# Kernel optimization log

Measured on AMD Instinct MI355X. Metric: run time of the kernel, lower is better.

Reference implementation:

```python
import jax, jax.numpy as jnp
import numpy as np

NEG = -1000000000.0

def setup_inputs() -> dict:
    key = jax.random.key(0)
    kq, kk, kv = jax.random.split(key, 3)
    B, S, D = 4, 4096, 128
    q = jax.random.normal(kq, (B, S, D), dtype=jnp.float32)
    k = jax.random.normal(kk, (B, S, D), dtype=jnp.float32)
    v = jax.random.normal(kv, (B, S, D), dtype=jnp.float32)
    return {"q": q, "k": k, "v": v, "window_size": 128}

def reference(q, k, v, window_size):
    B, S, D = q.shape
    q = q / jnp.sqrt(jnp.asarray(D, q.dtype))
    # banded mask: keep |i-j| <= window_size-1 (tril(w-1) & triu(-(w-1)))
    idx = jnp.arange(S)
    band = jnp.abs(idx[:, None] - idx[None, :]) <= (window_size - 1)  # [S,S]
    scores = jnp.einsum('bqd,bkd->bqk', q, k)
    scores = jnp.where(band[None, :, :], scores, NEG)
    weights = jax.nn.softmax(scores, axis=-1)
    return jnp.einsum('bqk,bkd->bqd', weights, v)
```

## Files before the change

### kernel.cpp

```cpp
#include <hip/hip_runtime.h>

#define S_LEN  4096
#define D_DIM  128
#define MQ     64
#define KT     64
#define NBATCH 4

#define QS_STR 136
#define KS_STR 136
#define VT_STR 72
#define PS_STR 72

#define OFF_K0 8704
#define OFF_K1 17408
#define OFF_V0 26112
#define OFF_V1 36480
#define OFF_P  46848
#define LDS_TOT 56064

typedef __bf16 bf16x8 __attribute__((ext_vector_type(8)));
typedef float  f32x4  __attribute__((ext_vector_type(4)));
typedef unsigned short u16x4 __attribute__((ext_vector_type(4)));
typedef unsigned short u16x8 __attribute__((ext_vector_type(8)));

__device__ __forceinline__ unsigned short f2bf(float f) {
  return __builtin_bit_cast(unsigned short, static_cast<__bf16>(f));
}
__device__ __forceinline__ float fexp2(float x) { return __builtin_amdgcn_exp2f(x); }
__device__ __forceinline__ bf16x8 ld8(const unsigned short* p) {
  return __builtin_bit_cast(bf16x8, *(const u16x8*)p);
}
__device__ __forceinline__ f32x4 mfma16(bf16x8 a, bf16x8 b, f32x4 c) {
  return __builtin_amdgcn_mfma_f32_16x16x32_bf16(a, b, c, 0, 0, 0);
}

__global__ __launch_bounds__(512, 2)
void swa_fwd(const float* __restrict__ Qg, const float* __restrict__ Kg,
             const float* __restrict__ Vg, float* __restrict__ Og)
{
  __shared__ __align__(16) unsigned short lds[LDS_TOT];

  const int tid  = threadIdx.x;
  const int g    = (blockIdx.x & 7) * 32 + (blockIdx.x >> 3);
  const int b    = g >> 6;
  const int q0   = (g & 63) * MQ;
  const size_t base = (size_t)b * S_LEN * D_DIM;

  const int lane = tid & 63;
  const int wv   = tid >> 6;
  const int grp  = wv >> 2;
  const int wvg  = wv & 3;
  const int tg   = tid & 255;
  const int quad = lane >> 4;
  const int l15  = lane & 15;

  unsigned short* lds_q  = lds;
  unsigned short* lds_k  = lds + (grp ? OFF_K1 : OFF_K0);
  unsigned short* lds_vt = lds + (grp ? OFF_V1 : OFF_V0);
  unsigned short* pw     = lds + OFF_P + wv * 16 * PS_STR;

  const int t_lo = (q0 >= 128) ? 0 : (2 - (q0 >> 6));
  const int t_hi = (4032 - q0 >= 128) ? 4 : (2 + ((4032 - q0) >> 6));

  const int t_beg = grp ? 3 : t_lo;
  const int ntile = grp ? (t_hi - 2) : (3 - t_lo);

  const int vd0 = (tg & 31) * 4;
  const int vk0 = (tg >> 5) * 8;

  f32x4 qreg[8], kreg[8], vreg[8];
  if (grp == 0) {
    const float* gq = Qg + base + (size_t)q0 * D_DIM;
#pragma unroll
    for (int j = 0; j < 8; ++j) qreg[j] = *(const f32x4*)(gq + j * 1024 + tg * 4);
  }
  int kb = q0 + (t_beg - 2) * KT;
  if (ntile > 0) {
    const float* gk = Kg + base + (size_t)kb * D_DIM;
    const float* gv = Vg + base + (size_t)kb * D_DIM;
#pragma unroll
    for (int j = 0; j < 8; ++j) kreg[j] = *(const f32x4*)(gk + j * 1024 + tg * 4);
#pragma unroll
    for (int kk = 0; kk < 8; ++kk)
      vreg[kk] = *(const f32x4*)(gv + (size_t)(vk0 + kk) * D_DIM + vd0);
  }

  for (int s = tg; s < 16 * VT_STR; s += 256)
    lds_vt[128 * VT_STR + s] = (s < VT_STR) ? (unsigned short)0x3F80 : (unsigned short)0;

  if (grp == 0) {
    const float qsc = 1.4426950408889634f * 0.08838834764831845f;
#pragma unroll
    for (int j = 0; j < 8; ++j) {
      const int f = j * 1024 + tg * 4;
      u16x4 y;
#pragma unroll
      for (int e = 0; e < 4; ++e) y[e] = f2bf(qreg[j][e] * qsc);
      *(u16x4*)&lds_q[(f >> 7) * QS_STR + (f & 127)] = y;
    }
  }
  if (ntile > 0) {
#pragma unroll
    for (int j = 0; j < 8; ++j) {
      const int f = j * 1024 + tg * 4;
      u16x4 y;
#pragma unroll
      for (int e = 0; e < 4; ++e) y[e] = f2bf(kreg[j][e]);
      *(u16x4*)&lds_k[(f >> 7) * KS_STR + (f & 127)] = y;
    }
#pragma unroll
    for (int e = 0; e < 4; ++e) {
      u16x8 y;
#pragma unroll
      for (int kk = 0; kk < 8; ++kk) y[kk] = f2bf(vreg[kk][e]);
      *(u16x8*)&lds_vt[(vd0 + e) * VT_STR + vk0] = y;
    }
  }
  __syncthreads();

  bf16x8 aq[4];
#pragma unroll
  for (int ks = 0; ks < 4; ++ks)
    aq[ks] = ld8(&lds_q[(wvg * 16 + l15) * QS_STR + ks * 32 + quad * 8]);

  f32x4 acc[9];
#pragma unroll
  for (int d = 0; d < 9; ++d) acc[d] = (f32x4){0.f, 0.f, 0.f, 0.f};

  for (int step = 0; step < 3; ++step) {
    const int t = t_beg + step;
    const bool cur = (step < ntile);
    const bool nxt = (step + 1 < ntile);

    if (nxt) {
      const float* gk = Kg + base + (size_t)(kb + KT) * D_DIM;
      const float* gv = Vg + base + (size_t)(kb + KT) * D_DIM;
#pragma unroll
      for (int j = 0; j < 8; ++j) kreg[j] = *(const f32x4*)(gk + j * 1024 + tg * 4);
#pragma unroll
      for (int kk = 0; kk < 8; ++kk)
        vreg[kk] = *(const f32x4*)(gv + (size_t)(vk0 + kk) * D_DIM + vd0);
    }

    if (cur) {
      int cbLo = 0, cbHi = 3;
      if (t == 0) cbLo = wvg;
      if (t == 4) cbHi = wvg;
      f32x4 sc[4];
      __builtin_amdgcn_s_setprio(1);
#pragma unroll
      for (int cb = 0; cb < 4; ++cb) {
        if (cb < cbLo || cb > cbHi) {
          sc[cb] = (f32x4){-1.0e30f, -1.0e30f, -1.0e30f, -1.0e30f};
          continue;
        }
        f32x4 a = (f32x4){0.f, 0.f, 0.f, 0.f};
#pragma unroll
        for (int ks = 0; ks < 4; ++ks) {
          const bf16x8 kf = ld8(&lds_k[(cb * 16 + l15) * KS_STR + ks * 32 + quad * 8]);
          a = mfma16(aq[ks], kf, a);
        }
        sc[cb] = a;
      }
      __builtin_amdgcn_s_setprio(0);

      if (t == 0 || t == 4) {
        const int off = (t - 2) * KT;
#pragma unroll
        for (int cb = 0; cb < 4; ++cb)
#pragma unroll
          for (int r = 0; r < 4; ++r) {
            const int delta = (wvg * 16 + quad * 4 + r) - (off + cb * 16 + l15);
            if (delta > 127 || delta < -127) sc[cb][r] = -1.0e30f;
          }
      }

#pragma unroll
      for (int cb = 0; cb < 4; ++cb)
#pragma unroll
        for (int r = 0; r < 4; ++r)
          sc[cb][r] = fexp2(sc[cb][r]);

#pragma unroll
      for (int cb = 0; cb < 4; ++cb)
#pragma unroll
        for (int r = 0; r < 4; ++r)
          pw[(quad * 4 + r) * PS_STR + cb * 16 + l15] = f2bf(sc[cb][r]);

      __builtin_amdgcn_s_setprio(1);
#pragma unroll
      for (int ks2 = 0; ks2 < 2; ++ks2) {
        const bf16x8 pf = ld8(&pw[l15 * PS_STR + ks2 * 32 + quad * 8]);
#pragma unroll
        for (int d = 0; d < 9; ++d) {
          const bf16x8 vf = ld8(&lds_vt[(d * 16 + l15) * VT_STR + ks2 * 32 + quad * 8]);
          acc[d] = mfma16(pf, vf, acc[d]);
        }
      }
      __builtin_amdgcn_s_setprio(0);
    }

    __syncthreads();
    if (nxt) {
#pragma unroll
      for (int j = 0; j < 8; ++j) {
        const int f = j * 1024 + tg * 4;
        u16x4 y;
#pragma unroll
        for (int e = 0; e < 4; ++e) y[e] = f2bf(kreg[j][e]);
        *(u16x4*)&lds_k[(f >> 7) * KS_STR + (f & 127)] = y;
      }
#pragma unroll
      for (int e = 0; e < 4; ++e) {
        u16x8 y;
#pragma unroll
        for (int kk = 0; kk < 8; ++kk) y[kk] = f2bf(vreg[kk][e]);
        *(u16x8*)&lds_vt[(vd0 + e) * VT_STR + vk0] = y;
      }
    }
    __syncthreads();
    kb += KT;
  }

  float* msc = (float*)lds;
  if (grp == 1) {
    float* p = msc + (wvg * 64 + lane) * 37;
#pragma unroll
    for (int d = 0; d < 9; ++d)
#pragma unroll
      for (int r = 0; r < 4; ++r) p[d * 4 + r] = acc[d][r];
  }
  __syncthreads();
  if (grp == 0) {
    const float* p = msc + (wvg * 64 + lane) * 37;
#pragma unroll
    for (int d = 0; d < 9; ++d)
#pragma unroll
      for (int r = 0; r < 4; ++r) acc[d][r] += p[d * 4 + r];

    float inv[4];
#pragma unroll
    for (int r = 0; r < 4; ++r) {
      const float lr = __shfl(acc[8][r], lane & 48, 64);
      inv[r] = 1.0f / lr;
    }
    float* go = Og + base + (size_t)q0 * D_DIM;
#pragma unroll
    for (int d = 0; d < 8; ++d)
#pragma unroll
      for (int r = 0; r < 4; ++r)
        go[(size_t)(wvg * 16 + quad * 4 + r) * D_DIM + d * 16 + l15] = acc[d][r] * inv[r];
  }
}

extern "C" void kernel_launch(void* const* d_in, const int* in_sizes, int n_in,
                              void* d_out, int out_size, void* d_ws, size_t ws_size,
                              hipStream_t stream) {
  const float* q = (const float*)d_in[0];
  const float* k = (const float*)d_in[1];
  const float* v = (const float*)d_in[2];
  float* o = (float*)d_out;
  dim3 grid(NBATCH * (S_LEN / MQ));
  dim3 block(512);
  swa_fwd<<<grid, block, 0, stream>>>(q, k, v, o);
}
```

Before: 86.01 us.

## Split into bf16 prep pass and small-block attention kernel reading from global

Result: slower. 98.47 us (+14.5%).

```diff
diff --git a/kernel.cpp b/kernel.cpp
--- a/kernel.cpp
+++ b/kernel.cpp
@@ -2,21 +2,12 @@
 
 #define S_LEN  4096
 #define D_DIM  128
-#define MQ     64
-#define KT     64
 #define NBATCH 4
-
-#define QS_STR 136
-#define KS_STR 136
-#define VT_STR 72
 #define PS_STR 72
 
-#define OFF_K0 8704
-#define OFF_K1 17408
-#define OFF_V0 26112
-#define OFF_V1 36480
-#define OFF_P  46848
-#define LDS_TOT 56064
+#define WS_Q 0
+#define WS_K 4194304
+#define WS_V 8388608
 
 typedef __bf16 bf16x8 __attribute__((ext_vector_type(8)));
 typedef float  f32x4  __attribute__((ext_vector_type(4)));
@@ -34,205 +25,167 @@
   return __builtin_amdgcn_mfma_f32_16x16x32_bf16(a, b, c, 0, 0, 0);
 }
 
-__global__ __launch_bounds__(512, 2)
-void swa_fwd(const float* __restrict__ Qg, const float* __restrict__ Kg,
-             const float* __restrict__ Vg, float* __restrict__ Og)
+__global__ __launch_bounds__(256, 4)
+void prep(const float* __restrict__ Q, const float* __restrict__ K,
+          const float* __restrict__ V, unsigned short* __restrict__ Qb,
+          unsigned short* __restrict__ Kb, unsigned short* __restrict__ Vt)
 {
-  __shared__ __align__(16) unsigned short lds[LDS_TOT];
+  __shared__ __align__(16) float lv[64 * 136];
+  const int t  = threadIdx.x;
+  const int b  = blockIdx.x >> 6;
+  const int s0 = (blockIdx.x & 63) * 64;
+  const size_t ibase = (size_t)b * S_LEN * D_DIM + (size_t)s0 * D_DIM;
+  const float qsc = 1.4426950408889634f * 0.08838834764831845f;
+
+#pragma unroll
+  for (int j = 0; j < 8; ++j) {
+    const int f = j * 1024 + t * 4;
+    const f32x4 xq = *(const f32x4*)(Q + ibase + f);
+    const f32x4 xk = *(const f32x4*)(K + ibase + f);
+    const f32x4 xv = *(const f32x4*)(V + ibase + f);
+    u16x4 yq, yk;
+#pragma unroll
+    for (int e = 0; e < 4; ++e) { yq[e] = f2bf(xq[e] * qsc); yk[e] = f2bf(xk[e]); }
+    *(u16x4*)(Qb + ibase + f) = yq;
+    *(u16x4*)(Kb + ibase + f) = yk;
+    *(f32x4*)&lv[(f >> 7) * 136 + (f & 127)] = xv;
+  }
+  __syncthreads();
+
+  const int d  = t >> 1;
+  const int ch = (t & 1) * 32;
+  unsigned short* out = Vt + ((size_t)b * 144 + d) * S_LEN + s0 + ch;
+#pragma unroll
+  for (int kk = 0; kk < 4; ++kk) {
+    u16x8 y;
+#pragma unroll
+    for (int e = 0; e < 8; ++e) y[e] = f2bf(lv[(ch + kk * 8 + e) * 136 + d]);
+    *(u16x8*)(out + kk * 8) = y;
+  }
+  if (t < 128) {
+    const int row = 128 + (t >> 3), k8 = (t & 7) * 8;
+    const unsigned short vv = (row == 128) ? (unsigned short)0x3F80 : (unsigned short)0;
+    u16x8 y;
+#pragma unroll
+    for (int e = 0; e < 8; ++e) y[e] = vv;
+    *(u16x8*)(Vt + ((size_t)b * 144 + row) * S_LEN + s0 + k8) = y;
+  }
+}
+
+__global__ __launch_bounds__(128, 2)
+void swa_fwd(const unsigned short* __restrict__ Qb, const unsigned short* __restrict__ Kb,
+             const unsigned short* __restrict__ Vt, float* __restrict__ Og)
+{
+  __shared__ __align__(16) unsigned short lds_p[2 * 16 * PS_STR];
+  __shared__ __align__(16) float msc[64 * 37];
 
   const int tid  = threadIdx.x;
-  const int g    = (blockIdx.x & 7) * 32 + (blockIdx.x >> 3);
-  const int b    = g >> 6;
-  const int q0   = (g & 63) * MQ;
-  const size_t base = (size_t)b * S_LEN * D_DIM;
-
   const int lane = tid & 63;
-  const int wv   = tid >> 6;
-  const int grp  = wv >> 2;
-  const int wvg  = wv & 3;
-  const int tg   = tid & 255;
+  const int part = tid >> 6;
   const int quad = lane >> 4;
   const int l15  = lane & 15;
 
-  unsigned short* lds_q  = lds;
-  unsigned short* lds_k  = lds + (grp ? OFF_K1 : OFF_K0);
-  unsigned short* lds_vt = lds + (grp ? OFF_V1 : OFF_V0);
-  unsigned short* pw     = lds + OFF_P + wv * 16 * PS_STR;
-
-  const int t_lo = (q0 >= 128) ? 0 : (2 - (q0 >> 6));
-  const int t_hi = (4032 - q0 >= 128) ? 4 : (2 + ((4032 - q0) >> 6));
-
-  const int t_beg = grp ? 3 : t_lo;
-  const int ntile = grp ? (t_hi - 2) : (3 - t_lo);
-
-  const int vd0 = (tg & 31) * 4;
-  const int vk0 = (tg >> 5) * 8;
-
-  f32x4 qreg[8], kreg[8], vreg[8];
-  if (grp == 0) {
-    const float* gq = Qg + base + (size_t)q0 * D_DIM;
-#pragma unroll
-    for (int j = 0; j < 8; ++j) qreg[j] = *(const f32x4*)(gq + j * 1024 + tg * 4);
-  }
-  int kb = q0 + (t_beg - 2) * KT;
-  if (ntile > 0) {
-    const float* gk = Kg + base + (size_t)kb * D_DIM;
-    const float* gv = Vg + base + (size_t)kb * D_DIM;
-#pragma unroll
-    for (int j = 0; j < 8; ++j) kreg[j] = *(const f32x4*)(gk + j * 1024 + tg * 4);
-#pragma unroll
-    for (int kk = 0; kk < 8; ++kk)
-      vreg[kk] = *(const f32x4*)(gv + (size_t)(vk0 + kk) * D_DIM + vd0);
-  }
-
-  for (int s = tg; s < 16 * VT_STR; s += 256)
-    lds_vt[128 * VT_STR + s] = (s < VT_STR) ? (unsigned short)0x3F80 : (unsigned short)0;
-
-  if (grp == 0) {
-    const float qsc = 1.4426950408889634f * 0.08838834764831845f;
-#pragma unroll
-    for (int j = 0; j < 8; ++j) {
-      const int f = j * 1024 + tg * 4;
-      u16x4 y;
-#pragma unroll
-      for (int e = 0; e < 4; ++e) y[e] = f2bf(qreg[j][e] * qsc);
-      *(u16x4*)&lds_q[(f >> 7) * QS_STR + (f & 127)] = y;
-    }
-  }
-  if (ntile > 0) {
-#pragma unroll
-    for (int j = 0; j < 8; ++j) {
-      const int f = j * 1024 + tg * 4;
-      u16x4 y;
-#pragma unroll
-      for (int e = 0; e < 4; ++e) y[e] = f2bf(kreg[j][e]);
-      *(u16x4*)&lds_k[(f >> 7) * KS_STR + (f & 127)] = y;
-    }
-#pragma unroll
-    for (int e = 0; e < 4; ++e) {
-      u16x8 y;
-#pragma unroll
-      for (int kk = 0; kk < 8; ++kk) y[kk] = f2bf(vreg[kk][e]);
-      *(u16x8*)&lds_vt[(vd0 + e) * VT_STR + vk0] = y;
-    }
+  const int g  = (blockIdx.x & 7) * 128 + (blockIdx.x >> 3);
+  const int b  = g >> 8;
+  const int qs = (g & 255) * 16;
+
+  const unsigned short* Qg = Qb + (size_t)b * S_LEN * D_DIM;
+  const unsigned short* Kg = Kb + (size_t)b * S_LEN * D_DIM;
+  const unsigned short* Vg = Vt + (size_t)b * 144 * S_LEN;
+
+  int lo_key = qs - 127; if (lo_key < 0) lo_key = 0;
+  int hi_key = qs + 142; if (hi_key > S_LEN - 1) hi_key = S_LEN - 1;
+  const int kb_lo = lo_key & ~63;
+  const int nt = (((hi_key & ~63) - kb_lo) >> 6) + 1;
+  const int n0 = nt >> 1;
+  const int tb = part ? n0 : 0;
+  const int te = part ? nt : n0;
+
+  bf16x8 aq[4];
+#pragma unroll
+  for (int ks = 0; ks < 4; ++ks)
+    aq[ks] = ld8(Qg + (size_t)(qs + l15) * D_DIM + ks * 32 + quad * 8);
+
+  f32x4 acc[9];
+#pragma unroll
+  for (int d = 0; d < 9; ++d) acc[d] = (f32x4){0.f, 0.f, 0.f, 0.f};
+
+  unsigned short* pw = lds_p + part * 16 * PS_STR;
+
+  for (int ti = tb; ti < te; ++ti) {
+    const int kb = kb_lo + ti * 64;
+
+    f32x4 sc[4];
+    __builtin_amdgcn_s_setprio(1);
+#pragma unroll
+    for (int cb = 0; cb < 4; ++cb) {
+      const int kbc = kb + cb * 16;
+      if (kbc + 15 < qs - 127 || kbc > qs + 142) {
+        sc[cb] = (f32x4){-1.0e30f, -1.0e30f, -1.0e30f, -1.0e30f};
+        continue;
+      }
+      f32x4 a = (f32x4){0.f, 0.f, 0.f, 0.f};
+#pragma unroll
+      for (int ks = 0; ks < 4; ++ks) {
+        const bf16x8 kf = ld8(Kg + (size_t)(kbc + l15) * D_DIM + ks * 32 + quad * 8);
+        a = mfma16(aq[ks], kf, a);
+      }
+      sc[cb] = a;
+    }
+    __builtin_amdgcn_s_setprio(0);
+
+    bf16x8 vfr[9];
+#pragma unroll
+    for (int d = 0; d < 9; ++d)
+      vfr[d] = ld8(Vg + (size_t)(d * 16 + l15) * S_LEN + kb + quad * 8);
+
+    if (kb < qs - 112 || kb > qs + 64) {
+#pragma unroll
+      for (int cb = 0; cb < 4; ++cb)
+#pragma unroll
+        for (int r = 0; r < 4; ++r) {
+          const int delta = (qs + quad * 4 + r) - (kb + cb * 16 + l15);
+          if (delta > 127 || delta < -127) sc[cb][r] = -1.0e30f;
+        }
+    }
+
+#pragma unroll
+    for (int cb = 0; cb < 4; ++cb)
+#pragma unroll
+      for (int r = 0; r < 4; ++r)
+        sc[cb][r] = fexp2(sc[cb][r]);
+
+#pragma unroll
+    for (int cb = 0; cb < 4; ++cb)
+#pragma unroll
+      for (int r = 0; r < 4; ++r)
+        pw[(quad * 4 + r) * PS_STR + cb * 16 + l15] = f2bf(sc[cb][r]);
+
+    __builtin_amdgcn_s_setprio(1);
+    {
+      const bf16x8 pf0 = ld8(&pw[l15 * PS_STR + quad * 8]);
+#pragma unroll
+      for (int d = 0; d < 9; ++d) acc[d] = mfma16(pf0, vfr[d], acc[d]);
+      const bf16x8 pf1 = ld8(&pw[l15 * PS_STR + 32 + quad * 8]);
+#pragma unroll
+      for (int d = 0; d < 9; ++d) {
+        const bf16x8 vf = ld8(Vg + (size_t)(d * 16 + l15) * S_LEN + kb + 32 + quad * 8);
+        acc[d] = mfma16(pf1, vf, acc[d]);
+      }
+    }
+    __builtin_amdgcn_s_setprio(0);
+  }
+
+  if (part == 1) {
+    float* p = msc + lane * 37;
+#pragma unroll
+    for (int d = 0; d < 9; ++d)
+#pragma unroll
+      for (int r = 0; r < 4; ++r) p[d * 4 + r] = acc[d][r];
   }
   __syncthreads();
-
-  bf16x8 aq[4];
-#pragma unroll
-  for (int ks = 0; ks < 4; ++ks)
-    aq[ks] = ld8(&lds_q[(wvg * 16 + l15) * QS_STR + ks * 32 + quad * 8]);
-
-  f32x4 acc[9];
-#pragma unroll
-  for (int d = 0; d < 9; ++d) acc[d] = (f32x4){0.f, 0.f, 0.f, 0.f};
-
-  for (int step = 0; step < 3; ++step) {
-    const int t = t_beg + step;
-    const bool cur = (step < ntile);
-    const bool nxt = (step + 1 < ntile);
-
-    if (nxt) {
-      const float* gk = Kg + base + (size_t)(kb + KT) * D_DIM;
-      const float* gv = Vg + base + (size_t)(kb + KT) * D_DIM;
-#pragma unroll
-      for (int j = 0; j < 8; ++j) kreg[j] = *(const f32x4*)(gk + j * 1024 + tg * 4);
-#pragma unroll
-      for (int kk = 0; kk < 8; ++kk)
-        vreg[kk] = *(const f32x4*)(gv + (size_t)(vk0 + kk) * D_DIM + vd0);
-    }
-
-    if (cur) {
-      int cbLo = 0, cbHi = 3;
-      if (t == 0) cbLo = wvg;
-      if (t == 4) cbHi = wvg;
-      f32x4 sc[4];
-      __builtin_amdgcn_s_setprio(1);
-#pragma unroll
-      for (int cb = 0; cb < 4; ++cb) {
-        if (cb < cbLo || cb > cbHi) {
-          sc[cb] = (f32x4){-1.0e30f, -1.0e30f, -1.0e30f, -1.0e30f};
-          continue;
-        }
-        f32x4 a = (f32x4){0.f, 0.f, 0.f, 0.f};
-#pragma unroll
-        for (int ks = 0; ks < 4; ++ks) {
-          const bf16x8 kf = ld8(&lds_k[(cb * 16 + l15) * KS_STR + ks * 32 + quad * 8]);
-          a = mfma16(aq[ks], kf, a);
-        }
-        sc[cb] = a;
-      }
-      __builtin_amdgcn_s_setprio(0);
-
-      if (t == 0 || t == 4) {
-        const int off = (t - 2) * KT;
-#pragma unroll
-        for (int cb = 0; cb < 4; ++cb)
-#pragma unroll
-          for (int r = 0; r < 4; ++r) {
-            const int delta = (wvg * 16 + quad * 4 + r) - (off + cb * 16 + l15);
-            if (delta > 127 || delta < -127) sc[cb][r] = -1.0e30f;
-          }
-      }
-
-#pragma unroll
-      for (int cb = 0; cb < 4; ++cb)
-#pragma unroll
-        for (int r = 0; r < 4; ++r)
-          sc[cb][r] = fexp2(sc[cb][r]);
-
-#pragma unroll
-      for (int cb = 0; cb < 4; ++cb)
-#pragma unroll
-        for (int r = 0; r < 4; ++r)
-          pw[(quad * 4 + r) * PS_STR + cb * 16 + l15] = f2bf(sc[cb][r]);
-
-      __builtin_amdgcn_s_setprio(1);
-#pragma unroll
-      for (int ks2 = 0; ks2 < 2; ++ks2) {
-        const bf16x8 pf = ld8(&pw[l15 * PS_STR + ks2 * 32 + quad * 8]);
-#pragma unroll
-        for (int d = 0; d < 9; ++d) {
-          const bf16x8 vf = ld8(&lds_vt[(d * 16 + l15) * VT_STR + ks2 * 32 + quad * 8]);
-          acc[d] = mfma16(pf, vf, acc[d]);
-        }
-      }
-      __builtin_amdgcn_s_setprio(0);
-    }
-
-    __syncthreads();
-    if (nxt) {
-#pragma unroll
-      for (int j = 0; j < 8; ++j) {
-        const int f = j * 1024 + tg * 4;
-        u16x4 y;
-#pragma unroll
-        for (int e = 0; e < 4; ++e) y[e] = f2bf(kreg[j][e]);
-        *(u16x4*)&lds_k[(f >> 7) * KS_STR + (f & 127)] = y;
-      }
-#pragma unroll
-      for (int e = 0; e < 4; ++e) {
-        u16x8 y;
-#pragma unroll
-        for (int kk = 0; kk < 8; ++kk) y[kk] = f2bf(vreg[kk][e]);
-        *(u16x8*)&lds_vt[(vd0 + e) * VT_STR + vk0] = y;
-      }
-    }
-    __syncthreads();
-    kb += KT;
-  }
-
-  float* msc = (float*)lds;
-  if (grp == 1) {
-    float* p = msc + (wvg * 64 + lane) * 37;
-#pragma unroll
-    for (int d = 0; d < 9; ++d)
-#pragma unroll
-      for (int r = 0; r < 4; ++r) p[d * 4 + r] = acc[d][r];
-  }
-  __syncthreads();
-  if (grp == 0) {
-    const float* p = msc + (wvg * 64 + lane) * 37;
+  if (part == 0) {
+    const float* p = msc + lane * 37;
 #pragma unroll
     for (int d = 0; d < 9; ++d)
 #pragma unroll
@@ -244,12 +197,12 @@
       const float lr = __shfl(acc[8][r], lane & 48, 64);
       inv[r] = 1.0f / lr;
     }
-    float* go = Og + base + (size_t)q0 * D_DIM;
+    float* go = Og + ((size_t)b * S_LEN + qs) * D_DIM;
 #pragma unroll
     for (int d = 0; d < 8; ++d)
 #pragma unroll
       for (int r = 0; r < 4; ++r)
-        go[(size_t)(wvg * 16 + quad * 4 + r) * D_DIM + d * 16 + l15] = acc[d][r] * inv[r];
+        go[(size_t)(quad * 4 + r) * D_DIM + d * 16 + l15] = acc[d][r] * inv[r];
   }
 }
 
@@ -260,7 +213,10 @@
   const float* k = (const float*)d_in[1];
   const float* v = (const float*)d_in[2];
   float* o = (float*)d_out;
-  dim3 grid(NBATCH * (S_LEN / MQ));
-  dim3 block(512);
-  swa_fwd<<<grid, block, 0, stream>>>(q, k, v, o);
-}
+  unsigned short* qb = (unsigned short*)((char*)d_ws + WS_Q);
+  unsigned short* kb = (unsigned short*)((char*)d_ws + WS_K);
+  unsigned short* vt = (unsigned short*)((char*)d_ws + WS_V);
+
+  prep<<<dim3(NBATCH * (S_LEN / 64)), dim3(256), 0, stream>>>(q, k, v, qb, kb, vt);
+  swa_fwd<<<dim3(NBATCH * (S_LEN / 16)), dim3(128), 0, stream>>>(qb, kb, vt, o);
+}
```

## Double-buffer K/V tiles in swizzled LDS and load Q directly to registers

Applied to the files above, without the earlier changes.

New measurement: 89.30 us. 1.04x slower.

```diff
diff --git a/kernel.cpp b/kernel.cpp
--- a/kernel.cpp
+++ b/kernel.cpp
@@ -5,18 +5,13 @@
 #define MQ     64
 #define KT     64
 #define NBATCH 4
-
-#define QS_STR 136
-#define KS_STR 136
-#define VT_STR 72
 #define PS_STR 72
 
-#define OFF_K0 8704
-#define OFF_K1 17408
-#define OFF_V0 26112
-#define OFF_V1 36480
-#define OFF_P  46848
-#define LDS_TOT 56064
+#define KBYTES 16384
+#define VBYTES 16384
+#define OFF_VB 65536
+#define OFF_PB 131072
+#define LDS_TOT (131072 + 8 * 16 * PS_STR * 2)
 
 typedef __bf16 bf16x8 __attribute__((ext_vector_type(8)));
 typedef float  f32x4  __attribute__((ext_vector_type(4)));
@@ -27,7 +22,7 @@
   return __builtin_bit_cast(unsigned short, static_cast<__bf16>(f));
 }
 __device__ __forceinline__ float fexp2(float x) { return __builtin_amdgcn_exp2f(x); }
-__device__ __forceinline__ bf16x8 ld8(const unsigned short* p) {
+__device__ __forceinline__ bf16x8 ld8(const void* p) {
   return __builtin_bit_cast(bf16x8, *(const u16x8*)p);
 }
 __device__ __forceinline__ f32x4 mfma16(bf16x8 a, bf16x8 b, f32x4 c) {
@@ -38,7 +33,7 @@
 void swa_fwd(const float* __restrict__ Qg, const float* __restrict__ Kg,
              const float* __restrict__ Vg, float* __restrict__ Og)
 {
-  __shared__ __align__(16) unsigned short lds[LDS_TOT];
+  __shared__ __align__(16) unsigned char lds[LDS_TOT];
 
   const int tid  = threadIdx.x;
   const int g    = (blockIdx.x & 7) * 32 + (blockIdx.x >> 3);
@@ -53,94 +48,98 @@
   const int tg   = tid & 255;
   const int quad = lane >> 4;
   const int l15  = lane & 15;
-
-  unsigned short* lds_q  = lds;
-  unsigned short* lds_k  = lds + (grp ? OFF_K1 : OFF_K0);
-  unsigned short* lds_vt = lds + (grp ? OFF_V1 : OFF_V0);
-  unsigned short* pw     = lds + OFF_P + wv * 16 * PS_STR;
+  const int xorv = (l15 & 7) << 4;
+
+  unsigned char* kbase = lds + grp * 2 * KBYTES;
+  unsigned char* vbase = lds + OFF_VB + grp * 2 * VBYTES;
+  unsigned short* pw   = (unsigned short*)(lds + OFF_PB) + wv * 16 * PS_STR;
 
   const int t_lo = (q0 >= 128) ? 0 : (2 - (q0 >> 6));
   const int t_hi = (4032 - q0 >= 128) ? 4 : (2 + ((4032 - q0) >> 6));
-
-  const int t_beg = grp ? 3 : t_lo;
-  const int ntile = grp ? (t_hi - 2) : (3 - t_lo);
+  const int ns0 = 3 - t_lo, ns1 = t_hi - 2;
+  const int nsteps = ns0 > ns1 ? ns0 : ns1;
+  const int ntile  = grp ? ns1 : ns0;
+  const int t_beg  = grp ? 3 : t_lo;
+  const int kb0    = q0 + (t_beg - 2) * KT;
 
   const int vd0 = (tg & 31) * 4;
   const int vk0 = (tg >> 5) * 8;
-
-  f32x4 qreg[8], kreg[8], vreg[8];
-  if (grp == 0) {
-    const float* gq = Qg + base + (size_t)q0 * D_DIM;
-#pragma unroll
-    for (int j = 0; j < 8; ++j) qreg[j] = *(const f32x4*)(gq + j * 1024 + tg * 4);
-  }
-  int kb = q0 + (t_beg - 2) * KT;
+  const int krow0 = tg >> 5;
+  const int kcol  = ((tg & 31) * 8) ^ ((krow0 & 7) << 4);
+
+  f32x4 kreg[8], vreg[8];
   if (ntile > 0) {
-    const float* gk = Kg + base + (size_t)kb * D_DIM;
-    const float* gv = Vg + base + (size_t)kb * D_DIM;
+    const float* gk = Kg + base + (size_t)kb0 * D_DIM;
+    const float* gv = Vg + base + (size_t)kb0 * D_DIM;
 #pragma unroll
     for (int j = 0; j < 8; ++j) kreg[j] = *(const f32x4*)(gk + j * 1024 + tg * 4);
 #pragma unroll
     for (int kk = 0; kk < 8; ++kk)
       vreg[kk] = *(const f32x4*)(gv + (size_t)(vk0 + kk) * D_DIM + vd0);
   }
-
-  for (int s = tg; s < 16 * VT_STR; s += 256)
-    lds_vt[128 * VT_STR + s] = (s < VT_STR) ? (unsigned short)0x3F80 : (unsigned short)0;
-
-  if (grp == 0) {
+  bf16x8 aq[4];
+  {
     const float qsc = 1.4426950408889634f * 0.08838834764831845f;
+    const float* gq = Qg + base + (size_t)(q0 + wvg * 16 + l15) * D_DIM;
+#pragma unroll
+    for (int ks = 0; ks < 4; ++ks) {
+      const f32x4 a0 = *(const f32x4*)(gq + ks * 32 + quad * 8);
+      const f32x4 a1 = *(const f32x4*)(gq + ks * 32 + quad * 8 + 4);
+      u16x8 y;
+#pragma unroll
+      for (int e = 0; e < 4; ++e) { y[e] = f2bf(a0[e] * qsc); y[4 + e] = f2bf(a1[e] * qsc); }
+      aq[ks] = __builtin_bit_cast(bf16x8, y);
+    }
+  }
+
+  auto stage = [&](unsigned char* kd, unsigned char* vd) {
 #pragma unroll
     for (int j = 0; j < 8; ++j) {
-      const int f = j * 1024 + tg * 4;
       u16x4 y;
 #pragma unroll
-      for (int e = 0; e < 4; ++e) y[e] = f2bf(qreg[j][e] * qsc);
-      *(u16x4*)&lds_q[(f >> 7) * QS_STR + (f & 127)] = y;
-    }
-  }
-  if (ntile > 0) {
-#pragma unroll
-    for (int j = 0; j < 8; ++j) {
-      const int f = j * 1024 + tg * 4;
-      u16x4 y;
-#pragma unroll
       for (int e = 0; e < 4; ++e) y[e] = f2bf(kreg[j][e]);
-      *(u16x4*)&lds_k[(f >> 7) * KS_STR + (f & 127)] = y;
+      *(u16x4*)(kd + (j * 8 + krow0) * 256 + kcol) = y;
     }
 #pragma unroll
     for (int e = 0; e < 4; ++e) {
       u16x8 y;
 #pragma unroll
       for (int kk = 0; kk < 8; ++kk) y[kk] = f2bf(vreg[kk][e]);
-      *(u16x8*)&lds_vt[(vd0 + e) * VT_STR + vk0] = y;
-    }
-  }
-  __syncthreads();
-
-  bf16x8 aq[4];
-#pragma unroll
-  for (int ks = 0; ks < 4; ++ks)
-    aq[ks] = ld8(&lds_q[(wvg * 16 + l15) * QS_STR + ks * 32 + quad * 8]);
+      const int row = vd0 + e;
+      *(u16x8*)(vd + row * 128 + ((vk0 * 2) ^ ((row & 7) << 4))) = y;
+    }
+  };
+  if (ntile > 0) stage(kbase, vbase);
+  if (ntile > 1) {
+    const float* gk = Kg + base + (size_t)(kb0 + KT) * D_DIM;
+    const float* gv = Vg + base + (size_t)(kb0 + KT) * D_DIM;
+#pragma unroll
+    for (int j = 0; j < 8; ++j) kreg[j] = *(const f32x4*)(gk + j * 1024 + tg * 4);
+#pragma unroll
+    for (int kk = 0; kk < 8; ++kk)
+      vreg[kk] = *(const f32x4*)(gv + (size_t)(vk0 + kk) * D_DIM + vd0);
+  }
+  asm volatile("s_waitcnt lgkmcnt(0)" ::: "memory");
+  __builtin_amdgcn_s_barrier();
+  __builtin_amdgcn_sched_barrier(0);
 
   f32x4 acc[9];
 #pragma unroll
   for (int d = 0; d < 9; ++d) acc[d] = (f32x4){0.f, 0.f, 0.f, 0.f};
-
-  for (int step = 0; step < 3; ++step) {
-    const int t = t_beg + step;
+  bf16x8 vones;
+  {
+    u16x8 y;
+#pragma unroll
+    for (int e = 0; e < 8; ++e) y[e] = (l15 == 0) ? (unsigned short)0x3F80 : (unsigned short)0;
+    vones = __builtin_bit_cast(bf16x8, y);
+  }
+
+  for (int step = 0; step < nsteps; ++step) {
+    const int  t   = t_beg + step;
     const bool cur = (step < ntile);
     const bool nxt = (step + 1 < ntile);
-
-    if (nxt) {
-      const float* gk = Kg + base + (size_t)(kb + KT) * D_DIM;
-      const float* gv = Vg + base + (size_t)(kb + KT) * D_DIM;
-#pragma unroll
-      for (int j = 0; j < 8; ++j) kreg[j] = *(const f32x4*)(gk + j * 1024 + tg * 4);
-#pragma unroll
-      for (int kk = 0; kk < 8; ++kk)
-        vreg[kk] = *(const f32x4*)(gv + (size_t)(vk0 + kk) * D_DIM + vd0);
-    }
+    const unsigned char* kr = kbase + (step & 1) * KBYTES;
+    const unsigned char* vr = vbase + (step & 1) * VBYTES;
 
     if (cur) {
       int cbLo = 0, cbHi = 3;
@@ -157,7 +156,7 @@
         f32x4 a = (f32x4){0.f, 0.f, 0.f, 0.f};
 #pragma unroll
         for (int ks = 0; ks < 4; ++ks) {
-          const bf16x8 kf = ld8(&lds_k[(cb * 16 + l15) * KS_STR + ks * 32 + quad * 8]);
+          const bf16x8 kf = ld8(kr + (cb * 16 + l15) * 256 + ((ks * 64 + quad * 16) ^ xorv));
           a = mfma16(aq[ks], kf, a);
         }
         sc[cb] = a;
@@ -192,34 +191,30 @@
       for (int ks2 = 0; ks2 < 2; ++ks2) {
         const bf16x8 pf = ld8(&pw[l15 * PS_STR + ks2 * 32 + quad * 8]);
 #pragma unroll
-        for (int d = 0; d < 9; ++d) {
-          const bf16x8 vf = ld8(&lds_vt[(d * 16 + l15) * VT_STR + ks2 * 32 + quad * 8]);
+        for (int d = 0; d < 8; ++d) {
+          const bf16x8 vf = ld8(vr + (d * 16 + l15) * 128 + ((ks2 * 64 + quad * 16) ^ xorv));
           acc[d] = mfma16(pf, vf, acc[d]);
         }
+        acc[8] = mfma16(pf, vones, acc[8]);
       }
       __builtin_amdgcn_s_setprio(0);
     }
 
-    __syncthreads();
     if (nxt) {
-#pragma unroll
-      for (int j = 0; j < 8; ++j) {
-        const int f = j * 1024 + tg * 4;
-        u16x4 y;
-#pragma unroll
-        for (int e = 0; e < 4; ++e) y[e] = f2bf(kreg[j][e]);
-        *(u16x4*)&lds_k[(f >> 7) * KS_STR + (f & 127)] = y;
-      }
-#pragma unroll
-      for (int e = 0; e < 4; ++e) {
-        u16x8 y;
-#pragma unroll
-        for (int kk = 0; kk < 8; ++kk) y[kk] = f2bf(vreg[kk][e]);
-        *(u16x8*)&lds_vt[(vd0 + e) * VT_STR + vk0] = y;
-      }
-    }
-    __syncthreads();
-    kb += KT;
+      stage(kbase + ((step + 1) & 1) * KBYTES, vbase + ((step + 1) & 1) * VBYTES);
+      if (step + 2 < ntile) {
+        const float* gk = Kg + base + (size_t)(kb0 + (step + 2) * KT) * D_DIM;
+        const float* gv = Vg + base + (size_t)(kb0 + (step + 2) * KT) * D_DIM;
+#pragma unroll
+        for (int j = 0; j < 8; ++j) kreg[j] = *(const f32x4*)(gk + j * 1024 + tg * 4);
+#pragma unroll
+        for (int kk = 0; kk < 8; ++kk)
+          vreg[kk] = *(const f32x4*)(gv + (size_t)(vk0 + kk) * D_DIM + vd0);
+      }
+    }
+    asm volatile("s_waitcnt lgkmcnt(0)" ::: "memory");
+    __builtin_amdgcn_s_barrier();
+    __builtin_amdgcn_sched_barrier(0);
   }
 
   float* msc = (float*)lds;
```

## Halve query tile to 32 rows with 256-thread blocks and direct Q loads

Applied to the files above, without the earlier changes.

Result: no change. 87.37 us (+1.6%).

```diff
diff --git a/kernel.cpp b/kernel.cpp
--- a/kernel.cpp
+++ b/kernel.cpp
@@ -2,21 +2,19 @@
 
 #define S_LEN  4096
 #define D_DIM  128
-#define MQ     64
+#define MQ     32
 #define KT     64
 #define NBATCH 4
 
-#define QS_STR 136
 #define KS_STR 136
 #define VT_STR 72
 #define PS_STR 72
 
-#define OFF_K0 8704
-#define OFF_K1 17408
-#define OFF_V0 26112
-#define OFF_V1 36480
-#define OFF_P  46848
-#define LDS_TOT 56064
+#define OFF_K1 8704
+#define OFF_V0 17408
+#define OFF_V1 26624
+#define OFF_P  35840
+#define LDS_TOT 40448
 
 typedef __bf16 bf16x8 __attribute__((ext_vector_type(8)));
 typedef float  f32x4  __attribute__((ext_vector_type(4)));
@@ -34,123 +32,106 @@
   return __builtin_amdgcn_mfma_f32_16x16x32_bf16(a, b, c, 0, 0, 0);
 }
 
-__global__ __launch_bounds__(512, 2)
+__global__ __launch_bounds__(256, 2)
 void swa_fwd(const float* __restrict__ Qg, const float* __restrict__ Kg,
              const float* __restrict__ Vg, float* __restrict__ Og)
 {
   __shared__ __align__(16) unsigned short lds[LDS_TOT];
 
   const int tid  = threadIdx.x;
-  const int g    = (blockIdx.x & 7) * 32 + (blockIdx.x >> 3);
-  const int b    = g >> 6;
-  const int q0   = (g & 63) * MQ;
+  const int g    = (blockIdx.x & 7) * 64 + (blockIdx.x >> 3);
+  const int b    = g >> 7;
+  const int qs   = (g & 127) * MQ;
   const size_t base = (size_t)b * S_LEN * D_DIM;
 
   const int lane = tid & 63;
   const int wv   = tid >> 6;
-  const int grp  = wv >> 2;
-  const int wvg  = wv & 3;
-  const int tg   = tid & 255;
+  const int grp  = wv >> 1;
+  const int wg   = wv & 1;
+  const int tg   = tid & 127;
   const int quad = lane >> 4;
   const int l15  = lane & 15;
-
-  unsigned short* lds_q  = lds;
-  unsigned short* lds_k  = lds + (grp ? OFF_K1 : OFF_K0);
+  const int qsw  = qs + wg * 16;
+
+  unsigned short* lds_k  = lds + (grp ? OFF_K1 : 0);
   unsigned short* lds_vt = lds + (grp ? OFF_V1 : OFF_V0);
   unsigned short* pw     = lds + OFF_P + wv * 16 * PS_STR;
 
-  const int t_lo = (q0 >= 128) ? 0 : (2 - (q0 >> 6));
-  const int t_hi = (4032 - q0 >= 128) ? 4 : (2 + ((4032 - q0) >> 6));
-
-  const int t_beg = grp ? 3 : t_lo;
-  const int ntile = grp ? (t_hi - 2) : (3 - t_lo);
-
+  int lo = qs - 127; if (lo < 0) lo = 0;
+  int hi = qs + MQ + 126; if (hi > S_LEN - 1) hi = S_LEN - 1;
+  const int kb_lo = lo & ~63;
+  const int nt = (((hi & ~63) - kb_lo) >> 6) + 1;
+  const int n0 = nt >> 1, n1 = nt - n0;
+  const int ntile = grp ? n1 : n0;
+  const int tb    = grp ? n0 : 0;
+
+  const int vk0 = (tg >> 5) * 16;
   const int vd0 = (tg & 31) * 4;
-  const int vk0 = (tg >> 5) * 8;
-
-  f32x4 qreg[8], kreg[8], vreg[8];
-  if (grp == 0) {
-    const float* gq = Qg + base + (size_t)q0 * D_DIM;
-#pragma unroll
-    for (int j = 0; j < 8; ++j) qreg[j] = *(const f32x4*)(gq + j * 1024 + tg * 4);
-  }
-  int kb = q0 + (t_beg - 2) * KT;
-  if (ntile > 0) {
-    const float* gk = Kg + base + (size_t)kb * D_DIM;
-    const float* gv = Vg + base + (size_t)kb * D_DIM;
-#pragma unroll
-    for (int j = 0; j < 8; ++j) kreg[j] = *(const f32x4*)(gk + j * 1024 + tg * 4);
-#pragma unroll
-    for (int kk = 0; kk < 8; ++kk)
-      vreg[kk] = *(const f32x4*)(gv + (size_t)(vk0 + kk) * D_DIM + vd0);
-  }
-
-  for (int s = tg; s < 16 * VT_STR; s += 256)
-    lds_vt[128 * VT_STR + s] = (s < VT_STR) ? (unsigned short)0x3F80 : (unsigned short)0;
-
-  if (grp == 0) {
+
+  bf16x8 aq[4];
+  {
     const float qsc = 1.4426950408889634f * 0.08838834764831845f;
-#pragma unroll
-    for (int j = 0; j < 8; ++j) {
-      const int f = j * 1024 + tg * 4;
-      u16x4 y;
-#pragma unroll
-      for (int e = 0; e < 4; ++e) y[e] = f2bf(qreg[j][e] * qsc);
-      *(u16x4*)&lds_q[(f >> 7) * QS_STR + (f & 127)] = y;
-    }
-  }
-  if (ntile > 0) {
-#pragma unroll
-    for (int j = 0; j < 8; ++j) {
-      const int f = j * 1024 + tg * 4;
-      u16x4 y;
-#pragma unroll
-      for (int e = 0; e < 4; ++e) y[e] = f2bf(kreg[j][e]);
-      *(u16x4*)&lds_k[(f >> 7) * KS_STR + (f & 127)] = y;
-    }
-#pragma unroll
-    for (int e = 0; e < 4; ++e) {
+    const float* gq = Qg + base + (size_t)(qsw + l15) * D_DIM;
+#pragma unroll
+    for (int ks = 0; ks < 4; ++ks) {
+      const f32x4 a0 = *(const f32x4*)(gq + ks * 32 + quad * 8);
+      const f32x4 a1 = *(const f32x4*)(gq + ks * 32 + quad * 8 + 4);
       u16x8 y;
 #pragma unroll
-      for (int kk = 0; kk < 8; ++kk) y[kk] = f2bf(vreg[kk][e]);
-      *(u16x8*)&lds_vt[(vd0 + e) * VT_STR + vk0] = y;
-    }
-  }
-  __syncthreads();
-
-  bf16x8 aq[4];
-#pragma unroll
-  for (int ks = 0; ks < 4; ++ks)
-    aq[ks] = ld8(&lds_q[(wvg * 16 + l15) * QS_STR + ks * 32 + quad * 8]);
+      for (int e = 0; e < 4; ++e) { y[e] = f2bf(a0[e] * qsc); y[4 + e] = f2bf(a1[e] * qsc); }
+      aq[ks] = __builtin_bit_cast(bf16x8, y);
+    }
+  }
 
   f32x4 acc[9];
 #pragma unroll
   for (int d = 0; d < 9; ++d) acc[d] = (f32x4){0.f, 0.f, 0.f, 0.f};
-
-  for (int step = 0; step < 3; ++step) {
-    const int t = t_beg + step;
+  bf16x8 vones;
+  {
+    u16x8 y;
+#pragma unroll
+    for (int e = 0; e < 8; ++e) y[e] = (l15 == 0) ? (unsigned short)0x3F80 : (unsigned short)0;
+    vones = __builtin_bit_cast(bf16x8, y);
+  }
+
+  for (int step = 0; step < n1; ++step) {
     const bool cur = (step < ntile);
-    const bool nxt = (step + 1 < ntile);
-
-    if (nxt) {
-      const float* gk = Kg + base + (size_t)(kb + KT) * D_DIM;
-      const float* gv = Vg + base + (size_t)(kb + KT) * D_DIM;
-#pragma unroll
-      for (int j = 0; j < 8; ++j) kreg[j] = *(const f32x4*)(gk + j * 1024 + tg * 4);
-#pragma unroll
-      for (int kk = 0; kk < 8; ++kk)
-        vreg[kk] = *(const f32x4*)(gv + (size_t)(vk0 + kk) * D_DIM + vd0);
-    }
+    const int  kb  = kb_lo + (tb + step) * KT;
 
     if (cur) {
-      int cbLo = 0, cbHi = 3;
-      if (t == 0) cbLo = wvg;
-      if (t == 4) cbHi = wvg;
+      const float* gk = Kg + base + (size_t)kb * D_DIM;
+#pragma unroll
+      for (int j = 0; j < 16; ++j) {
+        const int f = j * 512 + tg * 4;
+        const f32x4 x = *(const f32x4*)(gk + f);
+        u16x4 y;
+#pragma unroll
+        for (int e = 0; e < 4; ++e) y[e] = f2bf(x[e]);
+        *(u16x4*)&lds_k[(f >> 7) * KS_STR + (f & 127)] = y;
+      }
+      const float* gv = Vg + base + (size_t)kb * D_DIM;
+      f32x4 vx[16];
+#pragma unroll
+      for (int kk = 0; kk < 16; ++kk)
+        vx[kk] = *(const f32x4*)(gv + (size_t)(vk0 + kk) * D_DIM + vd0);
+#pragma unroll
+      for (int e = 0; e < 4; ++e) {
+        u16x8 y0, y1;
+#pragma unroll
+        for (int kk = 0; kk < 8; ++kk) { y0[kk] = f2bf(vx[kk][e]); y1[kk] = f2bf(vx[8 + kk][e]); }
+        *(u16x8*)&lds_vt[(vd0 + e) * VT_STR + vk0] = y0;
+        *(u16x8*)&lds_vt[(vd0 + e) * VT_STR + vk0 + 8] = y1;
+      }
+    }
+    __syncthreads();
+
+    if (cur) {
       f32x4 sc[4];
       __builtin_amdgcn_s_setprio(1);
 #pragma unroll
       for (int cb = 0; cb < 4; ++cb) {
-        if (cb < cbLo || cb > cbHi) {
+        const int kbc = kb + cb * 16;
+        if (kbc < qsw - 142 || kbc > qsw + 142) {
           sc[cb] = (f32x4){-1.0e30f, -1.0e30f, -1.0e30f, -1.0e30f};
           continue;
         }
@@ -164,15 +145,16 @@
       }
       __builtin_amdgcn_s_setprio(0);
 
-      if (t == 0 || t == 4) {
-        const int off = (t - 2) * KT;
-#pragma unroll
-        for (int cb = 0; cb < 4; ++cb)
+#pragma unroll
+      for (int cb = 0; cb < 4; ++cb) {
+        const int kbc = kb + cb * 16;
+        if (kbc < qsw - 112 || kbc > qsw + 112) {
 #pragma unroll
           for (int r = 0; r < 4; ++r) {
-            const int delta = (wvg * 16 + quad * 4 + r) - (off + cb * 16 + l15);
+            const int delta = (qsw + quad * 4 + r) - (kbc + l15);
             if (delta > 127 || delta < -127) sc[cb][r] = -1.0e30f;
           }
+        }
       }
 
 #pragma unroll
@@ -192,39 +174,20 @@
       for (int ks2 = 0; ks2 < 2; ++ks2) {
         const bf16x8 pf = ld8(&pw[l15 * PS_STR + ks2 * 32 + quad * 8]);
 #pragma unroll
-        for (int d = 0; d < 9; ++d) {
+        for (int d = 0; d < 8; ++d) {
           const bf16x8 vf = ld8(&lds_vt[(d * 16 + l15) * VT_STR + ks2 * 32 + quad * 8]);
           acc[d] = mfma16(pf, vf, acc[d]);
         }
+        acc[8] = mfma16(pf, vones, acc[8]);
       }
       __builtin_amdgcn_s_setprio(0);
     }
-
     __syncthreads();
-    if (nxt) {
-#pragma unroll
-      for (int j = 0; j < 8; ++j) {
-        const int f = j * 1024 + tg * 4;
-        u16x4 y;
-#pragma unroll
-        for (int e = 0; e < 4; ++e) y[e] = f2bf(kreg[j][e]);
-        *(u16x4*)&lds_k[(f >> 7) * KS_STR + (f & 127)] = y;
-      }
-#pragma unroll
-      for (int e = 0; e < 4; ++e) {
-        u16x8 y;
-#pragma unroll
-        for (int kk = 0; kk < 8; ++kk) y[kk] = f2bf(vreg[kk][e]);
-        *(u16x8*)&lds_vt[(vd0 + e) * VT_STR + vk0] = y;
-      }
-    }
-    __syncthreads();
-    kb += KT;
   }
 
   float* msc = (float*)lds;
   if (grp == 1) {
-    float* p = msc + (wvg * 64 + lane) * 37;
+    float* p = msc + (wg * 64 + lane) * 37;
 #pragma unroll
     for (int d = 0; d < 9; ++d)
 #pragma unroll
@@ -232,7 +195,7 @@
   }
   __syncthreads();
   if (grp == 0) {
-    const float* p = msc + (wvg * 64 + lane) * 37;
+    const float* p = msc + (wg * 64 + lane) * 37;
 #pragma unroll
     for (int d = 0; d < 9; ++d)
 #pragma unroll
@@ -244,12 +207,12 @@
       const float lr = __shfl(acc[8][r], lane & 48, 64);
       inv[r] = 1.0f / lr;
     }
-    float* go = Og + base + (size_t)q0 * D_DIM;
+    float* go = Og + base + (size_t)qsw * D_DIM;
 #pragma unroll
     for (int d = 0; d < 8; ++d)
 #pragma unroll
       for (int r = 0; r < 4; ++r)
-        go[(size_t)(wvg * 16 + quad * 4 + r) * D_DIM + d * 16 + l15] = acc[d][r] * inv[r];
+        go[(size_t)(quad * 4 + r) * D_DIM + d * 16 + l15] = acc[d][r] * inv[r];
   }
 }
 
@@ -261,6 +224,6 @@
   const float* v = (const float*)d_in[2];
   float* o = (float*)d_out;
   dim3 grid(NBATCH * (S_LEN / MQ));
-  dim3 block(512);
+  dim3 block(256);
   swa_fwd<<<grid, block, 0, stream>>>(q, k, v, o);
 }
```
